# Optimization experiments

Measured on AMD Instinct MI355X. Metric: run time of the kernel, lower is better.

The kernel has to match this reference:

```python
import jax, jax.numpy as jnp
import numpy as np
import math

DT_SCALE = 1.0
DT_MIN, DT_MAX = 0.001, 0.1


def setup_inputs() -> dict:
    key = jax.random.key(0)
    ku, kdt, ka, kb, kc = jax.random.split(key, 5)
    batch, seq_len, d_model, d_state = 32, 4096, 256, 64
    u = jax.random.normal(ku, (batch, seq_len, d_model), dtype=jnp.float32)
    # log_dt ~ U[log(dt_min), log(dt_max)]
    log_dt = jax.random.uniform(kdt, (d_model,), dtype=jnp.float32) * (
        math.log(DT_MAX) - math.log(DT_MIN)) + math.log(DT_MIN)
    # A_real = -exp(U(-1, 1))  (strictly negative -> stable recurrence)
    A_real = -jnp.exp(jax.random.uniform(ka, (d_model, d_state), dtype=jnp.float32) * 2.0 - 1.0)
    B = jax.random.normal(kb, (d_model, d_state), dtype=jnp.float32)
    C = jax.random.normal(kc, (d_model, d_state), dtype=jnp.float32)
    x0 = jnp.zeros((d_model, d_state), dtype=jnp.float32)
    return {"u": u, "log_dt": log_dt, "A_real": A_real, "B": B, "C": C, "x0": x0}


def reference(u, log_dt, A_real, B, C, x0):
    # u: (batch, seq_len, d_model)
    batch = u.shape[0]
    dt = jnp.exp(log_dt) * DT_SCALE                      # (D,)
    A_tilde = jnp.exp(A_real * dt[:, None])              # (D, N)
    B_tilde = (1.0 - A_tilde) * B / A_real               # (D, N)
    x_init = jnp.broadcast_to(x0, (batch,) + x0.shape)   # (B, D, N)

    def step(x, u_t):
        # x: (B, D, N), u_t: (B, D)
        x = A_tilde * x + B_tilde * u_t[..., None]
        y = jnp.sum(C * x, axis=-1)                      # (B, D)
        return x, y

    u_t_major = jnp.swapaxes(u, 0, 1)                    # (L, B, D)
    _, ys = jax.lax.scan(step, x_init, u_t_major)        # ys: (L, B, D)
    return jnp.swapaxes(ys, 0, 1)                        # (B, L, D)
```

## Files before the change

### kernel.cpp

```cpp
#include <hip/hip_runtime.h>
#include <math.h>

#define BATCH 32
#define SEQ   4096
#define DM    256
#define NS    64
#define TSTEP 16


__global__ __launch_bounds__(256, 2)
void pass1_kernel(const float* __restrict__ u,
                  const float* __restrict__ log_dt,
                  const float* __restrict__ A_real,
                  float* __restrict__ S, int Tc) {
    __shared__ float tiles[4][2][TSTEP][16];
    int wid  = threadIdx.x >> 6;
    int lane = threadIdx.x & 63;
    int wave = (blockIdx.x * blockDim.x + threadIdx.x) >> 6;
    int w  = wave & 511;
    int g  = wave >> 9;
    int b  = w >> 4;
    int d0 = (w & 15) << 4;
    int c   = lane >> 2;
    int sub = lane & 3;
    int d   = d0 + c;
    int n0  = sub << 4;

    float a[16], z[16];
    {
        float dt = expf(log_dt[d]);
        const float* Ap = A_real + d * NS + n0;
#pragma unroll
        for (int k = 0; k < 16; ++k) {
            a[k] = expf(Ap[k] * dt);
            z[k] = 0.0f;
        }
    }

    const float* gsrc = u + (size_t)b * SEQ * DM + (size_t)(g * Tc) * DM
                        + (size_t)(lane >> 2) * DM + d0 + ((lane & 3) << 2);
    const size_t tadv = (size_t)TSTEP * DM;
    float* slot0 = &tiles[wid][0][0][0] + (lane << 2);
    const int ntiles = Tc / TSTEP;

    float4 rnext = *(const float4*)gsrc;
    *(float4*)slot0 = rnext;
    gsrc += tadv;
    rnext = *(const float4*)gsrc;
    gsrc += tadv;

    for (int tile = 0; tile < ntiles; ++tile) {
        int cur = tile & 1;
        if (tile + 1 < ntiles)
            *(float4*)(slot0 + (((tile + 1) & 1) << 8)) = rnext;
        if (tile + 2 < ntiles) {
            rnext = *(const float4*)gsrc;
            gsrc += tadv;
        }
        const float* tb = &tiles[wid][cur][0][0] + c;
#pragma unroll
        for (int s = 0; s < TSTEP; ++s) {
            float uv = tb[s << 4];
#pragma unroll
            for (int k = 0; k < 16; ++k)
                z[k] = fmaf(a[k], z[k], uv);
        }
    }

    float* Sp = S + (((size_t)g * BATCH + b) * DM + d) * NS + n0;
    float4* Sp4 = (float4*)Sp;
#pragma unroll
    for (int j = 0; j < 4; ++j)
        Sp4[j] = make_float4(z[4 * j], z[4 * j + 1], z[4 * j + 2], z[4 * j + 3]);
}

__global__ void pass2_kernel(float* __restrict__ S,
                             const float* __restrict__ log_dt,
                             const float* __restrict__ A_real,
                             const float* __restrict__ B,
                             const float* __restrict__ x0,
                             int C, int Tc) {
    int idx = blockIdx.x * blockDim.x + threadIdx.x;
    if (idx >= BATCH * DM * NS) return;
    int dn = idx & (DM * NS - 1);
    int d = dn >> 6;
    float ar = A_real[dn];
    float dt = expf(log_dt[d]);
    float aT = expf(ar * dt * (float)Tc);
    float x0v = x0[dn];
    float prev;
    if (x0v == 0.0f) {
        prev = 0.0f;
    } else {
        float at = expf(ar * dt);
        float bt = (1.0f - at) * B[dn] / ar;
        prev = (bt != 0.0f) ? (x0v / bt) : 0.0f;
    }
    const size_t stride = (size_t)BATCH * DM * NS;
    if (C == 16) {
        float v[15];
#pragma unroll
        for (int g = 0; g < 15; ++g) v[g] = S[(size_t)g * stride + idx];
#pragma unroll
        for (int g = 0; g < 15; ++g) {
            S[(size_t)g * stride + idx] = prev;
            prev = fmaf(aT, prev, v[g]);
        }
        S[15 * stride + idx] = prev;
    } else {
        for (int g = 0; g < C - 1; ++g) {
            float* p = S + (size_t)g * stride + idx;
            float s = *p;
            *p = prev;
            prev = fmaf(aT, prev, s);
        }
        S[(size_t)(C - 1) * stride + idx] = prev;
    }
}

__global__ __launch_bounds__(256, 2)
void pass3_kernel(const float* __restrict__ u,
                  const float* __restrict__ log_dt,
                  const float* __restrict__ A_real,
                  const float* __restrict__ B,
                  const float* __restrict__ Cm,
                  const float* __restrict__ S,
                  const float* __restrict__ x0,
                  float* __restrict__ y, int Tc, int useS) {
    __shared__ float tiles[4][2][TSTEP][16];
    int wid  = threadIdx.x >> 6;
    int lane = threadIdx.x & 63;
    int wave = (blockIdx.x * blockDim.x + threadIdx.x) >> 6;
    int w  = wave & 511;
    int g  = wave >> 9;
    int b  = w >> 4;
    int d0 = (w & 15) << 4;
    int c   = lane >> 2;
    int sub = lane & 3;
    int d   = d0 + c;
    int n0  = sub << 4;

    float a[16], cbt[16], z[16];
    {
        float dt = expf(log_dt[d]);
        const float* Ap = A_real + d * NS + n0;
        const float* Bp = B + d * NS + n0;
        const float* Cp = Cm + d * NS + n0;
#pragma unroll
        for (int k = 0; k < 16; ++k) {
            float ar = Ap[k];
            float at = expf(ar * dt);
            a[k] = at;
            cbt[k] = Cp[k] * ((1.0f - at) * Bp[k] / ar);
        }
        if (useS) {
            const float4* Sp4 = (const float4*)(S +
                (((size_t)g * BATCH + b) * DM + d) * NS + n0);
#pragma unroll
            for (int j = 0; j < 4; ++j) {
                float4 v = Sp4[j];
                z[4 * j] = v.x; z[4 * j + 1] = v.y;
                z[4 * j + 2] = v.z; z[4 * j + 3] = v.w;
            }
        } else {
            const float* Xp = x0 + d * NS + n0;
#pragma unroll
            for (int k = 0; k < 16; ++k) {
                float x0v = Xp[k];
                if (x0v == 0.0f) { z[k] = 0.0f; }
                else {
                    float bt = (1.0f - a[k]) * Bp[k] / Ap[k];
                    z[k] = (bt != 0.0f) ? (x0v / bt) : 0.0f;
                }
            }
        }
    }

    const float* gsrc = u + (size_t)b * SEQ * DM + (size_t)(g * Tc) * DM
                        + (size_t)(lane >> 2) * DM + d0 + ((lane & 3) << 2);
    const size_t tadv = (size_t)TSTEP * DM;
    float* slot0 = &tiles[wid][0][0][0] + (lane << 2);
    const int ntiles = Tc / TSTEP;
    float* yptr = y + (size_t)b * SEQ * DM + (size_t)(g * Tc) * DM + d;

    float4 rnext = *(const float4*)gsrc;
    *(float4*)slot0 = rnext;
    gsrc += tadv;
    rnext = *(const float4*)gsrc;
    gsrc += tadv;

    for (int tile = 0; tile < ntiles; ++tile) {
        int cur = tile & 1;
        if (tile + 1 < ntiles)
            *(float4*)(slot0 + (((tile + 1) & 1) << 8)) = rnext;
        if (tile + 2 < ntiles) {
            rnext = *(const float4*)gsrc;
            gsrc += tadv;
        }
        const float* tb = &tiles[wid][cur][0][0] + c;
#pragma unroll
        for (int s = 0; s < TSTEP; ++s) {
            float uv = tb[s << 4];
            float p0 = 0.0f, p1 = 0.0f;
#pragma unroll
            for (int k = 0; k < 16; k += 2) {
                z[k]     = fmaf(a[k],     z[k],     uv); p0 = fmaf(cbt[k],     z[k],     p0);
                z[k + 1] = fmaf(a[k + 1], z[k + 1], uv); p1 = fmaf(cbt[k + 1], z[k + 1], p1);
            }
            float p = p0 + p1;
            p += __shfl_xor(p, 1);
            p += __shfl_xor(p, 2);
            if (sub == 0) *yptr = p;
            yptr += DM;
        }
    }
}

extern "C" void kernel_launch(void* const* d_in, const int* in_sizes, int n_in,
                              void* d_out, int out_size, void* d_ws, size_t ws_size,
                              hipStream_t stream) {
    const float* u      = (const float*)d_in[0];
    const float* log_dt = (const float*)d_in[1];
    const float* A_real = (const float*)d_in[2];
    const float* B      = (const float*)d_in[3];
    const float* Cm     = (const float*)d_in[4];
    const float* x0     = (const float*)d_in[5];
    float* y = (float*)d_out;
    float* S = (float*)d_ws;

    const size_t per_chunk = (size_t)BATCH * DM * NS * sizeof(float);
    int C = 16;
    while (C > 1 && (size_t)C * per_chunk > ws_size) C >>= 1;
    if ((size_t)C * per_chunk > ws_size) C = 1;
    int Tc = SEQ / C;

    if (C > 1) {
        pass1_kernel<<<dim3((C - 1) * 128), dim3(256), 0, stream>>>(
            u, log_dt, A_real, S, Tc);
        pass2_kernel<<<dim3((BATCH * DM * NS) / 256), dim3(256), 0, stream>>>(
            S, log_dt, A_real, B, x0, C, Tc);
    }
    pass3_kernel<<<dim3(C * 128), dim3(256), 0, stream>>>(
        u, log_dt, A_real, B, Cm, S, x0, y, Tc, (C > 1) ? 1 : 0);
}
```

Measured before the change: 388.4 us.

## Fuse chunk-0 output emission into the chunk-state pass and enlarge time tile

The first pass now also runs the full output scan for chunk 0, starting from x0, in 128 extra blocks. This work needs no carried state, so pass 3 only processes chunks 1..C-1 and less of it sits on the critical path after pass 2. The time tile is doubled from 16 to 32 steps, with two float4 loads per lane per tile, which raises LDS use and register pressure. With C=1 the fused kernel alone produces all of y.

```diff
diff --git a/kernel.cpp b/kernel.cpp
--- a/kernel.cpp
+++ b/kernel.cpp
@@ -5,20 +5,26 @@
 #define SEQ   4096
 #define DM    256
 #define NS    64
-#define TSTEP 16
+#define TSTEP 32
 
 
 __global__ __launch_bounds__(256, 2)
-void pass1_kernel(const float* __restrict__ u,
+void passA_kernel(const float* __restrict__ u,
                   const float* __restrict__ log_dt,
                   const float* __restrict__ A_real,
-                  float* __restrict__ S, int Tc) {
+                  const float* __restrict__ B,
+                  const float* __restrict__ Cm,
+                  float* __restrict__ S,
+                  const float* __restrict__ x0,
+                  float* __restrict__ y, int Tc) {
     __shared__ float tiles[4][2][TSTEP][16];
     int wid  = threadIdx.x >> 6;
     int lane = threadIdx.x & 63;
-    int wave = (blockIdx.x * blockDim.x + threadIdx.x) >> 6;
+    bool emit = (blockIdx.x < 128);
+    int wave, g;
+    if (emit) { wave = (blockIdx.x << 2) | wid;         g = 0; }
+    else      { wave = ((blockIdx.x - 128) << 2) | wid; g = wave >> 9; }
     int w  = wave & 511;
-    int g  = wave >> 9;
     int b  = w >> 4;
     int d0 = (w & 15) << 4;
     int c   = lane >> 2;
@@ -26,52 +32,107 @@
     int d   = d0 + c;
     int n0  = sub << 4;
 
+    float dt = expf(log_dt[d]);
+    const float* Ap = A_real + d * NS + n0;
     float a[16], z[16];
-    {
-        float dt = expf(log_dt[d]);
-        const float* Ap = A_real + d * NS + n0;
-#pragma unroll
-        for (int k = 0; k < 16; ++k) {
-            a[k] = expf(Ap[k] * dt);
-            z[k] = 0.0f;
-        }
-    }
-
+#pragma unroll
+    for (int k = 0; k < 16; ++k)
+        a[k] = expf(Ap[k] * dt);
+
+    const size_t tadv = (size_t)TSTEP * DM;
+    const size_t half = (size_t)16 * DM;
+    float* slotA = &tiles[wid][0][0][0] + (lane << 2);
+    const int ntiles = Tc / TSTEP;
     const float* gsrc = u + (size_t)b * SEQ * DM + (size_t)(g * Tc) * DM
                         + (size_t)(lane >> 2) * DM + d0 + ((lane & 3) << 2);
-    const size_t tadv = (size_t)TSTEP * DM;
-    float* slot0 = &tiles[wid][0][0][0] + (lane << 2);
-    const int ntiles = Tc / TSTEP;
-
-    float4 rnext = *(const float4*)gsrc;
-    *(float4*)slot0 = rnext;
-    gsrc += tadv;
-    rnext = *(const float4*)gsrc;
-    gsrc += tadv;
-
-    for (int tile = 0; tile < ntiles; ++tile) {
-        int cur = tile & 1;
-        if (tile + 1 < ntiles)
-            *(float4*)(slot0 + (((tile + 1) & 1) << 8)) = rnext;
-        if (tile + 2 < ntiles) {
-            rnext = *(const float4*)gsrc;
+
+    if (!emit) {
+#pragma unroll
+        for (int k = 0; k < 16; ++k) z[k] = 0.0f;
+        float4 rC = *(const float4*)gsrc;
+        float4 rD = *(const float4*)(gsrc + half);
+        *(float4*)slotA = rC;
+        *(float4*)(slotA + 256) = rD;
+        rC = *(const float4*)(gsrc + tadv);
+        rD = *(const float4*)(gsrc + tadv + half);
+        gsrc += 2 * tadv;
+        for (int t = 0; t < ntiles; ++t) {
+            if (t + 1 < ntiles) {
+                float* wp = slotA + (((t + 1) & 1) << 9);
+                *(float4*)wp = rC;
+                *(float4*)(wp + 256) = rD;
+            }
+            if (t + 2 < ntiles) {
+                rC = *(const float4*)gsrc;
+                rD = *(const float4*)(gsrc + half);
+                gsrc += tadv;
+            }
+            const float* tb = &tiles[wid][t & 1][0][0] + c;
+#pragma unroll
+            for (int s = 0; s < TSTEP; ++s) {
+                float uv = tb[s << 4];
+#pragma unroll
+                for (int k = 0; k < 16; ++k)
+                    z[k] = fmaf(a[k], z[k], uv);
+            }
+        }
+        float* Sp = S + (((size_t)g * BATCH + b) * DM + d) * NS + n0;
+        float4* Sp4 = (float4*)Sp;
+#pragma unroll
+        for (int j = 0; j < 4; ++j)
+            Sp4[j] = make_float4(z[4*j], z[4*j+1], z[4*j+2], z[4*j+3]);
+        return;
+    }
+
+    float cbt[16];
+    {
+        const float* Bp = B + d * NS + n0;
+        const float* Cp = Cm + d * NS + n0;
+        const float* Xp = x0 + d * NS + n0;
+#pragma unroll
+        for (int k = 0; k < 16; ++k) {
+            float bt = (1.0f - a[k]) * Bp[k] / Ap[k];
+            cbt[k] = Cp[k] * bt;
+            float x0v = Xp[k];
+            z[k] = (x0v == 0.0f) ? 0.0f : ((bt != 0.0f) ? (x0v / bt) : 0.0f);
+        }
+    }
+    float* yptr = y + (size_t)b * SEQ * DM + d;
+    float4 rC = *(const float4*)gsrc;
+    float4 rD = *(const float4*)(gsrc + half);
+    *(float4*)slotA = rC;
+    *(float4*)(slotA + 256) = rD;
+    rC = *(const float4*)(gsrc + tadv);
+    rD = *(const float4*)(gsrc + tadv + half);
+    gsrc += 2 * tadv;
+    for (int t = 0; t < ntiles; ++t) {
+        if (t + 1 < ntiles) {
+            float* wp = slotA + (((t + 1) & 1) << 9);
+            *(float4*)wp = rC;
+            *(float4*)(wp + 256) = rD;
+        }
+        if (t + 2 < ntiles) {
+            rC = *(const float4*)gsrc;
+            rD = *(const float4*)(gsrc + half);
             gsrc += tadv;
         }
-        const float* tb = &tiles[wid][cur][0][0] + c;
+        const float* tb = &tiles[wid][t & 1][0][0] + c;
 #pragma unroll
         for (int s = 0; s < TSTEP; ++s) {
             float uv = tb[s << 4];
-#pragma unroll
-            for (int k = 0; k < 16; ++k)
-                z[k] = fmaf(a[k], z[k], uv);
-        }
-    }
-
-    float* Sp = S + (((size_t)g * BATCH + b) * DM + d) * NS + n0;
-    float4* Sp4 = (float4*)Sp;
-#pragma unroll
-    for (int j = 0; j < 4; ++j)
-        Sp4[j] = make_float4(z[4 * j], z[4 * j + 1], z[4 * j + 2], z[4 * j + 3]);
+            float p0 = 0.0f, p1 = 0.0f;
+#pragma unroll
+            for (int k = 0; k < 16; k += 2) {
+                z[k]   = fmaf(a[k],   z[k],   uv); p0 = fmaf(cbt[k],   z[k],   p0);
+                z[k+1] = fmaf(a[k+1], z[k+1], uv); p1 = fmaf(cbt[k+1], z[k+1], p1);
+            }
+            float p = p0 + p1;
+            p += __shfl_xor(p, 1);
+            p += __shfl_xor(p, 2);
+            if (sub == 0) yptr[s * DM] = p;
+        }
+        yptr += tadv;
+    }
 }
 
 __global__ void pass2_kernel(float* __restrict__ S,
@@ -125,14 +186,13 @@
                   const float* __restrict__ B,
                   const float* __restrict__ Cm,
                   const float* __restrict__ S,
-                  const float* __restrict__ x0,
-                  float* __restrict__ y, int Tc, int useS) {
+                  float* __restrict__ y, int Tc) {
     __shared__ float tiles[4][2][TSTEP][16];
     int wid  = threadIdx.x >> 6;
     int lane = threadIdx.x & 63;
-    int wave = (blockIdx.x * blockDim.x + threadIdx.x) >> 6;
+    int wave = (blockIdx.x << 2) | wid;
+    int g  = 1 + (wave >> 9);
     int w  = wave & 511;
-    int g  = wave >> 9;
     int b  = w >> 4;
     int d0 = (w & 15) << 4;
     int c   = lane >> 2;
@@ -140,79 +200,70 @@
     int d   = d0 + c;
     int n0  = sub << 4;
 
+    float dt = expf(log_dt[d]);
+    const float* Ap = A_real + d * NS + n0;
     float a[16], cbt[16], z[16];
     {
-        float dt = expf(log_dt[d]);
-        const float* Ap = A_real + d * NS + n0;
         const float* Bp = B + d * NS + n0;
         const float* Cp = Cm + d * NS + n0;
 #pragma unroll
         for (int k = 0; k < 16; ++k) {
-            float ar = Ap[k];
-            float at = expf(ar * dt);
+            float at = expf(Ap[k] * dt);
             a[k] = at;
-            cbt[k] = Cp[k] * ((1.0f - at) * Bp[k] / ar);
-        }
-        if (useS) {
-            const float4* Sp4 = (const float4*)(S +
-                (((size_t)g * BATCH + b) * DM + d) * NS + n0);
-#pragma unroll
-            for (int j = 0; j < 4; ++j) {
-                float4 v = Sp4[j];
-                z[4 * j] = v.x; z[4 * j + 1] = v.y;
-                z[4 * j + 2] = v.z; z[4 * j + 3] = v.w;
-            }
-        } else {
-            const float* Xp = x0 + d * NS + n0;
-#pragma unroll
-            for (int k = 0; k < 16; ++k) {
-                float x0v = Xp[k];
-                if (x0v == 0.0f) { z[k] = 0.0f; }
-                else {
-                    float bt = (1.0f - a[k]) * Bp[k] / Ap[k];
-                    z[k] = (bt != 0.0f) ? (x0v / bt) : 0.0f;
-                }
-            }
-        }
-    }
-
+            cbt[k] = Cp[k] * ((1.0f - at) * Bp[k] / Ap[k]);
+        }
+        const float4* Sp4 = (const float4*)(S +
+            (((size_t)g * BATCH + b) * DM + d) * NS + n0);
+#pragma unroll
+        for (int j = 0; j < 4; ++j) {
+            float4 v = Sp4[j];
+            z[4*j] = v.x; z[4*j+1] = v.y; z[4*j+2] = v.z; z[4*j+3] = v.w;
+        }
+    }
+
+    const size_t tadv = (size_t)TSTEP * DM;
+    const size_t half = (size_t)16 * DM;
+    float* slotA = &tiles[wid][0][0][0] + (lane << 2);
+    const int ntiles = Tc / TSTEP;
     const float* gsrc = u + (size_t)b * SEQ * DM + (size_t)(g * Tc) * DM
                         + (size_t)(lane >> 2) * DM + d0 + ((lane & 3) << 2);
-    const size_t tadv = (size_t)TSTEP * DM;
-    float* slot0 = &tiles[wid][0][0][0] + (lane << 2);
-    const int ntiles = Tc / TSTEP;
     float* yptr = y + (size_t)b * SEQ * DM + (size_t)(g * Tc) * DM + d;
 
-    float4 rnext = *(const float4*)gsrc;
-    *(float4*)slot0 = rnext;
-    gsrc += tadv;
-    rnext = *(const float4*)gsrc;
-    gsrc += tadv;
-
-    for (int tile = 0; tile < ntiles; ++tile) {
-        int cur = tile & 1;
-        if (tile + 1 < ntiles)
-            *(float4*)(slot0 + (((tile + 1) & 1) << 8)) = rnext;
-        if (tile + 2 < ntiles) {
-            rnext = *(const float4*)gsrc;
+    float4 rC = *(const float4*)gsrc;
+    float4 rD = *(const float4*)(gsrc + half);
+    *(float4*)slotA = rC;
+    *(float4*)(slotA + 256) = rD;
+    rC = *(const float4*)(gsrc + tadv);
+    rD = *(const float4*)(gsrc + tadv + half);
+    gsrc += 2 * tadv;
+
+    for (int t = 0; t < ntiles; ++t) {
+        if (t + 1 < ntiles) {
+            float* wp = slotA + (((t + 1) & 1) << 9);
+            *(float4*)wp = rC;
+            *(float4*)(wp + 256) = rD;
+        }
+        if (t + 2 < ntiles) {
+            rC = *(const float4*)gsrc;
+            rD = *(const float4*)(gsrc + half);
             gsrc += tadv;
         }
-        const float* tb = &tiles[wid][cur][0][0] + c;
+        const float* tb = &tiles[wid][t & 1][0][0] + c;
 #pragma unroll
         for (int s = 0; s < TSTEP; ++s) {
             float uv = tb[s << 4];
             float p0 = 0.0f, p1 = 0.0f;
 #pragma unroll
             for (int k = 0; k < 16; k += 2) {
-                z[k]     = fmaf(a[k],     z[k],     uv); p0 = fmaf(cbt[k],     z[k],     p0);
-                z[k + 1] = fmaf(a[k + 1], z[k + 1], uv); p1 = fmaf(cbt[k + 1], z[k + 1], p1);
+                z[k]   = fmaf(a[k],   z[k],   uv); p0 = fmaf(cbt[k],   z[k],   p0);
+                z[k+1] = fmaf(a[k+1], z[k+1], uv); p1 = fmaf(cbt[k+1], z[k+1], p1);
             }
             float p = p0 + p1;
             p += __shfl_xor(p, 1);
             p += __shfl_xor(p, 2);
-            if (sub == 0) *yptr = p;
-            yptr += DM;
-        }
+            if (sub == 0) yptr[s * DM] = p;
+        }
+        yptr += tadv;
     }
 }
 
@@ -234,12 +285,12 @@
     if ((size_t)C * per_chunk > ws_size) C = 1;
     int Tc = SEQ / C;
 
+    passA_kernel<<<dim3(C * 128), dim3(256), 0, stream>>>(
+        u, log_dt, A_real, B, Cm, S, x0, y, Tc);
     if (C > 1) {
-        pass1_kernel<<<dim3((C - 1) * 128), dim3(256), 0, stream>>>(
-            u, log_dt, A_real, S, Tc);
         pass2_kernel<<<dim3((BATCH * DM * NS) / 256), dim3(256), 0, stream>>>(
             S, log_dt, A_real, B, x0, C, Tc);
-    }
-    pass3_kernel<<<dim3(C * 128), dim3(256), 0, stream>>>(
-        u, log_dt, A_real, B, Cm, S, x0, y, Tc, (C > 1) ? 1 : 0);
-}
+        pass3_kernel<<<dim3((C - 1) * 128), dim3(256), 0, stream>>>(
+            u, log_dt, A_real, B, Cm, S, y, Tc);
+    }
+}
```

Measured after the change: 402.7 us. +3.7%, slower.
